# Performance work log

Measured on AMD Instinct MI355X. Metric: run time of the kernel, lower is better.

The kernel has to match this reference:

```python
import jax, jax.numpy as jnp
import numpy as np

N = 80000      # nodes
E = 1280000    # edges
G = 64         # graphs in batch
CIN = 128
D = 64
NUM_LAYERS = 6


def setup_inputs() -> dict:
    key = jax.random.key(0)
    ks = jax.random.split(key, 12)
    s = 0.05
    return {
        "x": jax.random.normal(ks[0], (N, CIN), jnp.float32),
        "edge_index": jax.random.randint(ks[1], (2, E), 0, N, dtype=jnp.int32),
        "batch": jnp.sort(jax.random.randint(ks[2], (N,), 0, G, dtype=jnp.int32)),
        "W_in": jax.random.normal(ks[3], (CIN, D), jnp.float32) * s,
        "b_in": jnp.zeros((D,), jnp.float32),
        "W_hid": jax.random.normal(ks[4], (NUM_LAYERS - 1, D, D), jnp.float32) * s,
        "b_hid": jnp.zeros((NUM_LAYERS - 1, D), jnp.float32),
        "lin1_w": jax.random.normal(ks[5], (2 * D, 64), jnp.float32) * s,
        "lin1_b": jnp.zeros((64,), jnp.float32),
        "lin2_w": jax.random.normal(ks[6], (64, 64), jnp.float32) * s,
        "lin2_b": jnp.zeros((64,), jnp.float32),
        "lin3_w": jax.random.normal(ks[7], (64, 1), jnp.float32) * s,
        "lin3_b": jnp.zeros((1,), jnp.float32),
    }


def _gcn_norm(edge_index, n):
    # PyG gcn_norm: add self-loops, symmetric D^-1/2 (A+I) D^-1/2 normalization
    loops = jnp.arange(n, dtype=edge_index.dtype)
    src = jnp.concatenate([edge_index[0], loops])
    dst = jnp.concatenate([edge_index[1], loops])
    deg = jax.ops.segment_sum(jnp.ones_like(src, jnp.float32), dst, num_segments=n)
    dinv = jnp.where(deg > 0, jax.lax.rsqrt(jnp.maximum(deg, 1.0)), 0.0)
    norm = dinv[src] * dinv[dst]
    return src, dst, norm


def _gcn_conv(x, W, b, src, dst, norm, n):
    h = x @ W                                   # [N, D]
    msg = h[src] * norm[:, None]                # [E+N, D] gather + scale
    out = jax.ops.segment_sum(msg, dst, num_segments=n)
    return out + b


def reference(x, edge_index, batch, W_in, b_in, W_hid, b_hid,
              lin1_w, lin1_b, lin2_w, lin2_b, lin3_w, lin3_b):
    n = x.shape[0]
    src, dst, norm = _gcn_norm(edge_index, n)
    # layer 0: in_channels -> D, then ReLU
    h = jax.nn.relu(_gcn_conv(x, W_in, b_in, src, dst, norm, n))
    # hidden layers: ReLU on all but the last conv
    n_hid = W_hid.shape[0]
    for i in range(n_hid):
        h = _gcn_conv(h, W_hid[i], b_hid[i], src, dst, norm, n)
        if i != n_hid - 1:
            h = jax.nn.relu(h)
    # global add + max pooling per graph
    x1 = jax.ops.segment_sum(h, batch, num_segments=G)   # [G, D]
    x2 = jax.ops.segment_max(h, batch, num_segments=G)   # [G, D]
    g = jnp.concatenate([x1, x2], axis=1)                # [G, 2D]
    g = jax.nn.relu(g @ lin1_w + lin1_b)
    g = jax.nn.relu(g @ lin2_w + lin2_b)
    return g @ lin3_w + lin3_b                           # [G, 1]
```

## Files before the change

kernel.cpp:

```cpp
#include <hip/hip_runtime.h>
#include <hip/hip_bf16.h>
#include <cstdint>
#include <cstddef>


#define FEAT 64

typedef __bf16 bf16_t;
typedef bf16_t bf16x8 __attribute__((ext_vector_type(8)));
typedef float f32x4 __attribute__((ext_vector_type(4)));

static __device__ inline unsigned short f2bf(float f) {
  unsigned u = __float_as_uint(f);
  unsigned r = (u + 0x7FFF + ((u >> 16) & 1)) >> 16;
  return (unsigned short)r;
}
static __device__ inline float bf2f(unsigned short u) {
  return __uint_as_float(((unsigned)u) << 16);
}


__global__ __launch_bounds__(256) void init_kernel(int* deg, int* cursor,
    float* gsum, unsigned int* gmax, int n) {
  int i = blockIdx.x * 256 + threadIdx.x;
  if (i < n) { deg[i] = 0; cursor[i] = 0; }
  if (i < 64 * FEAT) { gsum[i] = 0.f; gmax[i] = 0xFF800000u; }
}

__global__ __launch_bounds__(256) void hist_kernel(const int* __restrict__ dst,
    int* __restrict__ deg, int e, int n) {
  const int slice = blockIdx.x & 7;
  const int lo = slice * (n >> 3);
  const int hi = lo + (n >> 3);
  const int nb = gridDim.x >> 3;
  const int bid = blockIdx.x >> 3;
  for (int i = bid * 256 + threadIdx.x; i < e; i += nb * 256) {
    int d = dst[i];
    if (d >= lo && d < hi) atomicAdd(&deg[d], 1);
  }
}

__global__ __launch_bounds__(256) void dinv_kernel(const int* __restrict__ deg,
    float* __restrict__ dinv, int n) {
  int i = blockIdx.x * 256 + threadIdx.x;
  if (i < n) dinv[i] = rsqrtf((float)(deg[i] + 1));
}

__global__ __launch_bounds__(256) void scan1_kernel(const int* __restrict__ deg,
    int* __restrict__ offs, int* __restrict__ bsums, int n) {
  __shared__ int buf[256];
  int t = threadIdx.x;
  int i = blockIdx.x * 256 + t;
  int v = (i < n) ? deg[i] : 0;
  buf[t] = v;
  __syncthreads();
  for (int off = 1; off < 256; off <<= 1) {
    int add = (t >= off) ? buf[t - off] : 0;
    __syncthreads();
    buf[t] += add;
    __syncthreads();
  }
  if (i < n) offs[i] = buf[t] - v;
  if (t == 255) bsums[blockIdx.x] = buf[255];
}

__global__ __launch_bounds__(512) void scan2_kernel(int* bs, int nb) {
  __shared__ int buf[512];
  int t = threadIdx.x;
  int v = (t < nb) ? bs[t] : 0;
  buf[t] = v;
  __syncthreads();
  for (int off = 1; off < 512; off <<= 1) {
    int add = (t >= off) ? buf[t - off] : 0;
    __syncthreads();
    buf[t] += add;
    __syncthreads();
  }
  if (t < nb) bs[t] = buf[t] - v;
}

__global__ __launch_bounds__(256) void scan3_kernel(int* __restrict__ offs,
    const int* __restrict__ bs, int n) {
  int i = blockIdx.x * 256 + threadIdx.x;
  if (i < n) offs[i] += bs[blockIdx.x];
}

__global__ __launch_bounds__(256) void fill_kernel(const int* __restrict__ src,
    const int* __restrict__ dst, const int* __restrict__ offs,
    int* __restrict__ cursor, int* __restrict__ csr_src, int e, int n) {
  const int slice = blockIdx.x & 7;
  const int lo = slice * (n >> 3);
  const int hi = lo + (n >> 3);
  const int nb = gridDim.x >> 3;
  const int bid = blockIdx.x >> 3;
  for (int i = bid * 256 + threadIdx.x; i < e; i += nb * 256) {
    int d = dst[i];
    if (d >= lo && d < hi) {
      int pos = offs[d] + atomicAdd(&cursor[d], 1);
      csr_src[pos] = src[i];
    }
  }
}

__global__ __launch_bounds__(256) void wprep_kernel(
    const float* __restrict__ W_in, const float* __restrict__ W_hid,
    unsigned short* __restrict__ wf0h, unsigned short* __restrict__ wf0l,
    unsigned short* __restrict__ wfhh, unsigned short* __restrict__ wfhl) {
  int tid = threadIdx.x;
  for (int i = tid; i < 16 * 64 * 8; i += 256) {
    int j = i & 7, l = (i >> 3) & 63, f = i >> 9;
    int q = f & 3, t = f >> 2;
    int k = q * 32 + (l >> 4) * 8 + j, c = t * 16 + (l & 15);
    float w = W_in[k * 64 + c];
    unsigned short hi = f2bf(w);
    wf0h[i] = hi;
    wf0l[i] = f2bf(w - bf2f(hi));
  }
  for (int i = tid; i < 5 * 8 * 64 * 8; i += 256) {
    int j = i & 7, l = (i >> 3) & 63, f = (i >> 9) & 7, m = i >> 12;
    int q = f & 1, t = f >> 1;
    int k = q * 32 + (l >> 4) * 8 + j, c = t * 16 + (l & 15);
    float w = W_hid[(m * 64 + k) * 64 + c];
    unsigned short hi = f2bf(w);
    wfhh[i] = hi;
    wfhl[i] = f2bf(w - bf2f(hi));
  }
}

static __device__ inline void split8(const float4& a, const float4& b,
                                     bf16x8& vh, bf16x8& vl) {
  union { unsigned short us[8]; bf16x8 v; } uh, ul;
  float va[8] = {a.x, a.y, a.z, a.w, b.x, b.y, b.z, b.w};
#pragma unroll
  for (int j = 0; j < 8; ++j) {
    unsigned short hi = f2bf(va[j]);
    uh.us[j] = hi;
    ul.us[j] = f2bf(va[j] - bf2f(hi));
  }
  vh = uh.v; vl = ul.v;
}

__global__ __launch_bounds__(256) void xform0_kernel(
    const float* __restrict__ x, const unsigned short* __restrict__ wf0h,
    const unsigned short* __restrict__ wf0l, const float* __restrict__ dinv,
    unsigned short* __restrict__ tg, int n) {
  const int lane = threadIdx.x & 63;
  const int r = lane & 15, g = lane >> 4;
  const int gw = (blockIdx.x * 256 + threadIdx.x) >> 6;
  const int th = gw & 1;
  const int tile = gw >> 1;
  if (tile >= (n >> 4)) return;

  bf16x8 wh[2][4], wl[2][4];
#pragma unroll
  for (int tt = 0; tt < 2; ++tt)
#pragma unroll
    for (int q = 0; q < 4; ++q) {
      int f = (th * 2 + tt) * 4 + q;
      wh[tt][q] = *reinterpret_cast<const bf16x8*>(&wf0h[(f * 64 + lane) * 8]);
      wl[tt][q] = *reinterpret_cast<const bf16x8*>(&wf0l[(f * 64 + lane) * 8]);
    }

  const int m0 = tile << 4;
  const float* xrow = x + (size_t)(m0 + r) * 128 + g * 8;
  f32x4 acc[2] = {{0.f, 0.f, 0.f, 0.f}, {0.f, 0.f, 0.f, 0.f}};
#pragma unroll
  for (int q = 0; q < 4; ++q) {
    float4 lo4 = *(const float4*)(xrow + q * 32);
    float4 hi4 = *(const float4*)(xrow + q * 32 + 4);
    bf16x8 ah, al;
    split8(lo4, hi4, ah, al);
#pragma unroll
    for (int tt = 0; tt < 2; ++tt) {
      acc[tt] = __builtin_amdgcn_mfma_f32_16x16x32_bf16(ah, wh[tt][q], acc[tt], 0, 0, 0);
      acc[tt] = __builtin_amdgcn_mfma_f32_16x16x32_bf16(al, wh[tt][q], acc[tt], 0, 0, 0);
      acc[tt] = __builtin_amdgcn_mfma_f32_16x16x32_bf16(ah, wl[tt][q], acc[tt], 0, 0, 0);
    }
  }
  float4 dv = *(const float4*)&dinv[m0 + g * 4];
  unsigned short* orow = tg + (size_t)m0 * 64;
#pragma unroll
  for (int tt = 0; tt < 2; ++tt) {
    int c = (th * 2 + tt) * 16 + r;
    orow[(g * 4 + 0) * 64 + c] = f2bf(acc[tt][0] * dv.x);
    orow[(g * 4 + 1) * 64 + c] = f2bf(acc[tt][1] * dv.y);
    orow[(g * 4 + 2) * 64 + c] = f2bf(acc[tt][2] * dv.z);
    orow[(g * 4 + 3) * 64 + c] = f2bf(acc[tt][3] * dv.w);
  }
}

__global__ __launch_bounds__(256) void xform_kernel(
    const float* __restrict__ h, const unsigned short* __restrict__ wflh,
    const unsigned short* __restrict__ wfll, const float* __restrict__ dinv,
    unsigned short* __restrict__ tg, int n) {
  const int lane = threadIdx.x & 63;
  const int r = lane & 15, g = lane >> 4;
  const int tile = (blockIdx.x * 256 + threadIdx.x) >> 6;
  if (tile >= (n >> 4)) return;

  bf16x8 wh[4][2], wl[4][2];
#pragma unroll
  for (int t = 0; t < 4; ++t)
#pragma unroll
    for (int q = 0; q < 2; ++q) {
      int f = t * 2 + q;
      wh[t][q] = *reinterpret_cast<const bf16x8*>(&wflh[(f * 64 + lane) * 8]);
      wl[t][q] = *reinterpret_cast<const bf16x8*>(&wfll[(f * 64 + lane) * 8]);
    }

  const int m0 = tile << 4;
  const float* hrow = h + (size_t)(m0 + r) * 64 + g * 8;
  f32x4 acc[4] = {{0.f, 0.f, 0.f, 0.f}, {0.f, 0.f, 0.f, 0.f},
                  {0.f, 0.f, 0.f, 0.f}, {0.f, 0.f, 0.f, 0.f}};
#pragma unroll
  for (int q = 0; q < 2; ++q) {
    float4 lo4 = *(const float4*)(hrow + q * 32);
    float4 hi4 = *(const float4*)(hrow + q * 32 + 4);
    bf16x8 ah, al;
    split8(lo4, hi4, ah, al);
#pragma unroll
    for (int t = 0; t < 4; ++t) {
      acc[t] = __builtin_amdgcn_mfma_f32_16x16x32_bf16(ah, wh[t][q], acc[t], 0, 0, 0);
      acc[t] = __builtin_amdgcn_mfma_f32_16x16x32_bf16(al, wh[t][q], acc[t], 0, 0, 0);
      acc[t] = __builtin_amdgcn_mfma_f32_16x16x32_bf16(ah, wl[t][q], acc[t], 0, 0, 0);
    }
  }
  float4 dv = *(const float4*)&dinv[m0 + g * 4];
  unsigned short* orow = tg + (size_t)m0 * 64;
#pragma unroll
  for (int t = 0; t < 4; ++t) {
    orow[(g * 4 + 0) * 64 + t * 16 + r] = f2bf(acc[t][0] * dv.x);
    orow[(g * 4 + 1) * 64 + t * 16 + r] = f2bf(acc[t][1] * dv.y);
    orow[(g * 4 + 2) * 64 + t * 16 + r] = f2bf(acc[t][2] * dv.z);
    orow[(g * 4 + 3) * 64 + t * 16 + r] = f2bf(acc[t][3] * dv.w);
  }
}

__global__ __launch_bounds__(256) void agg_mid_kernel(
    const unsigned short* __restrict__ tg_in, const int* __restrict__ csr_src,
    const int* __restrict__ offs, const int* __restrict__ cnt,
    const float* __restrict__ dinv, const float* __restrict__ bias,
    float* __restrict__ h_out, int n) {
  int v = (blockIdx.x * 256 + threadIdx.x) >> 6;
  int lane = threadIdx.x & 63;
  if (v >= n) return;
  float acc = bf2f(tg_in[(size_t)v * 64 + lane]);
  int j = offs[v];
  int end = j + cnt[v];
  for (; j + 7 < end; j += 8) {
    int s0 = csr_src[j + 0], s1 = csr_src[j + 1];
    int s2 = csr_src[j + 2], s3 = csr_src[j + 3];
    int s4 = csr_src[j + 4], s5 = csr_src[j + 5];
    int s6 = csr_src[j + 6], s7 = csr_src[j + 7];
    float t0 = bf2f(tg_in[(size_t)s0 * 64 + lane]);
    float t1 = bf2f(tg_in[(size_t)s1 * 64 + lane]);
    float t2 = bf2f(tg_in[(size_t)s2 * 64 + lane]);
    float t3 = bf2f(tg_in[(size_t)s3 * 64 + lane]);
    float t4 = bf2f(tg_in[(size_t)s4 * 64 + lane]);
    float t5 = bf2f(tg_in[(size_t)s5 * 64 + lane]);
    float t6 = bf2f(tg_in[(size_t)s6 * 64 + lane]);
    float t7 = bf2f(tg_in[(size_t)s7 * 64 + lane]);
    acc += ((t0 + t1) + (t2 + t3)) + ((t4 + t5) + (t6 + t7));
  }
  for (; j < end; ++j)
    acc += bf2f(tg_in[(size_t)csr_src[j] * 64 + lane]);
  h_out[(size_t)v * 64 + lane] = fmaxf(fmaf(dinv[v], acc, bias[lane]), 0.f);
}

__global__ __launch_bounds__(256) void agg_last_kernel(
    const unsigned short* __restrict__ tg_in, const int* __restrict__ csr_src,
    const int* __restrict__ offs, const int* __restrict__ cnt,
    const float* __restrict__ dinv, const float* __restrict__ bias,
    float* __restrict__ h, int n) {
  int v = (blockIdx.x * 256 + threadIdx.x) >> 6;
  int lane = threadIdx.x & 63;
  if (v >= n) return;
  float acc = bf2f(tg_in[(size_t)v * 64 + lane]);
  int j = offs[v];
  int end = j + cnt[v];
  for (; j + 7 < end; j += 8) {
    int s0 = csr_src[j + 0], s1 = csr_src[j + 1];
    int s2 = csr_src[j + 2], s3 = csr_src[j + 3];
    int s4 = csr_src[j + 4], s5 = csr_src[j + 5];
    int s6 = csr_src[j + 6], s7 = csr_src[j + 7];
    float t0 = bf2f(tg_in[(size_t)s0 * 64 + lane]);
    float t1 = bf2f(tg_in[(size_t)s1 * 64 + lane]);
    float t2 = bf2f(tg_in[(size_t)s2 * 64 + lane]);
    float t3 = bf2f(tg_in[(size_t)s3 * 64 + lane]);
    float t4 = bf2f(tg_in[(size_t)s4 * 64 + lane]);
    float t5 = bf2f(tg_in[(size_t)s5 * 64 + lane]);
    float t6 = bf2f(tg_in[(size_t)s6 * 64 + lane]);
    float t7 = bf2f(tg_in[(size_t)s7 * 64 + lane]);
    acc += ((t0 + t1) + (t2 + t3)) + ((t4 + t5) + (t6 + t7));
  }
  for (; j < end; ++j)
    acc += bf2f(tg_in[(size_t)csr_src[j] * 64 + lane]);
  h[(size_t)v * 64 + lane] = fmaf(dinv[v], acc, bias[lane]);
}


__device__ inline void atomic_max_float(float* addr, float val) {
  if (val >= 0.f)
    atomicMax((int*)addr, __float_as_int(val));
  else
    atomicMin((unsigned int*)addr, (unsigned int)__float_as_int(val));
}

#define POOL_CHUNK 128

__global__ __launch_bounds__(256) void pool_kernel(const float* __restrict__ h,
    const int* __restrict__ batch, float* __restrict__ gsum,
    float* __restrict__ gmax, int n) {
  int wave = (blockIdx.x * 256 + threadIdx.x) >> 6;
  int lane = threadIdx.x & 63;
  int start = wave * POOL_CHUNK;
  if (start >= n) return;
  int end = min(start + POOL_CHUNK, n);
  float s = 0.f, m = -INFINITY;
  int cur = batch[start];
  for (int v = start; v < end; ++v) {
    int g = batch[v];
    if (g != cur) {
      atomicAdd(&gsum[cur * 64 + lane], s);
      atomic_max_float(&gmax[cur * 64 + lane], m);
      s = 0.f; m = -INFINITY; cur = g;
    }
    float x = h[(size_t)v * 64 + lane];
    s += x;
    m = fmaxf(m, x);
  }
  atomicAdd(&gsum[cur * 64 + lane], s);
  atomic_max_float(&gmax[cur * 64 + lane], m);
}


__global__ __launch_bounds__(256) void mlp_kernel(const float* __restrict__ gsum,
    const float* __restrict__ gmax, const float* __restrict__ w1,
    const float* __restrict__ b1, const float* __restrict__ w2,
    const float* __restrict__ b2, const float* __restrict__ w3,
    const float* __restrict__ b3, float* __restrict__ out) {
  __shared__ float smem[64 * 128 + 64 * 64];
  float* gg = smem;
  float* z1 = smem + 64 * 128;
  int t = threadIdx.x;
  for (int i = t; i < 64 * 128; i += 256) {
    int g = i >> 7, f = i & 127;
    gg[i] = (f < 64) ? gsum[g * 64 + f] : gmax[g * 64 + (f - 64)];
  }
  __syncthreads();
  for (int i = t; i < 64 * 64; i += 256) {
    int g = i >> 6, j = i & 63;
    float acc = b1[j];
    for (int f = 0; f < 128; ++f) acc = fmaf(gg[(g << 7) + f], w1[f * 64 + j], acc);
    z1[i] = fmaxf(acc, 0.f);
  }
  __syncthreads();
  float* z2 = smem;
  for (int i = t; i < 64 * 64; i += 256) {
    int g = i >> 6, j = i & 63;
    float acc = b2[j];
    for (int f = 0; f < 64; ++f) acc = fmaf(z1[(g << 6) + f], w2[f * 64 + j], acc);
    z2[i] = fmaxf(acc, 0.f);
  }
  __syncthreads();
  if (t < 64) {
    float acc = b3[0];
    for (int j = 0; j < 64; ++j) acc = fmaf(z2[(t << 6) + j], w3[j], acc);
    out[t] = acc;
  }
}


extern "C" void kernel_launch(void* const* d_in, const int* in_sizes, int n_in,
                              void* d_out, int out_size, void* d_ws, size_t ws_size,
                              hipStream_t stream) {
  const float* x      = (const float*)d_in[0];
  const int*   eidx   = (const int*)d_in[1];
  const int*   batch  = (const int*)d_in[2];
  const float* W_in   = (const float*)d_in[3];
  const float* b_in   = (const float*)d_in[4];
  const float* W_hid  = (const float*)d_in[5];
  const float* b_hid  = (const float*)d_in[6];
  const float* lin1_w = (const float*)d_in[7];
  const float* lin1_b = (const float*)d_in[8];
  const float* lin2_w = (const float*)d_in[9];
  const float* lin2_b = (const float*)d_in[10];
  const float* lin3_w = (const float*)d_in[11];
  const float* lin3_b = (const float*)d_in[12];
  float* out = (float*)d_out;

  const int N = in_sizes[2];
  const int E = in_sizes[1] / 2;
  const int CIN = in_sizes[0] / N;
  const int n_hid = in_sizes[5] / (64 * 64);

  const int* src = eidx;
  const int* dst = eidx + E;

  char* ws = (char*)d_ws;
  size_t off = 0;
  auto alloc = [&](size_t bytes) {
    size_t o = off;
    off = (off + bytes + 255) & ~(size_t)255;
    return o;
  };
  int*            deg     = (int*)(ws + alloc((size_t)N * 4));
  int*            cursor  = (int*)(ws + alloc((size_t)N * 4));
  float*          dinv    = (float*)(ws + alloc((size_t)N * 4));
  int*            offs    = (int*)(ws + alloc((size_t)N * 4));
  int*            bsums   = (int*)(ws + alloc(1024 * 4));
  int*            csr_src = (int*)(ws + alloc((size_t)E * 4));
  unsigned short* tg_a    = (unsigned short*)(ws + alloc((size_t)N * 64 * 2));
  unsigned short* tg_b    = (unsigned short*)(ws + alloc((size_t)N * 64 * 2));
  float*          hbuf    = (float*)(ws + alloc((size_t)N * 64 * 4));
  unsigned short* wf0h    = (unsigned short*)(ws + alloc(16 * 64 * 8 * 2));
  unsigned short* wf0l    = (unsigned short*)(ws + alloc(16 * 64 * 8 * 2));
  unsigned short* wfhh    = (unsigned short*)(ws + alloc(5 * 8 * 64 * 8 * 2));
  unsigned short* wfhl    = (unsigned short*)(ws + alloc(5 * 8 * 64 * 8 * 2));
  float*          gsum    = (float*)(ws + alloc(64 * 64 * 4));
  float*          gmax    = (float*)(ws + alloc(64 * 64 * 4));
  (void)ws_size; (void)n_in; (void)out_size; (void)CIN;

  const int nbN = (N + 255) / 256;

  init_kernel<<<nbN, 256, 0, stream>>>(deg, cursor, gsum, (unsigned int*)gmax, N);
  hist_kernel<<<1024, 256, 0, stream>>>(dst, deg, E, N);
  dinv_kernel<<<nbN, 256, 0, stream>>>(deg, dinv, N);
  scan1_kernel<<<nbN, 256, 0, stream>>>(deg, offs, bsums, N);
  scan2_kernel<<<1, 512, 0, stream>>>(bsums, nbN);
  scan3_kernel<<<nbN, 256, 0, stream>>>(offs, bsums, N);
  fill_kernel<<<1024, 256, 0, stream>>>(src, dst, offs, cursor, csr_src, E, N);
  wprep_kernel<<<1, 256, 0, stream>>>(W_in, W_hid, wf0h, wf0l, wfhh, wfhl);

  const int agg_blocks = (N * 64 + 255) / 256;
  const int ntile = N >> 4;
  const int xf0_blocks = (ntile * 2 + 3) / 4;
  const int xf_blocks = (ntile + 3) / 4;

  xform0_kernel<<<xf0_blocks, 256, 0, stream>>>(x, wf0h, wf0l, dinv, tg_a, N);

  unsigned short* cur = tg_a;
  unsigned short* nxt = tg_b;
  for (int k = 0; k < n_hid; ++k) {
    const float* bias_k = (k == 0) ? b_in : (b_hid + (size_t)(k - 1) * 64);
    agg_mid_kernel<<<agg_blocks, 256, 0, stream>>>(
        cur, csr_src, offs, deg, dinv, bias_k, hbuf, N);
    xform_kernel<<<xf_blocks, 256, 0, stream>>>(
        hbuf, wfhh + (size_t)k * 8 * 64 * 8, wfhl + (size_t)k * 8 * 64 * 8,
        dinv, nxt, N);
    unsigned short* t = cur; cur = nxt; nxt = t;
  }
  agg_last_kernel<<<agg_blocks, 256, 0, stream>>>(
      cur, csr_src, offs, deg, dinv, b_hid + (size_t)(n_hid - 1) * 64, hbuf, N);

  const int pool_waves = (N + POOL_CHUNK - 1) / POOL_CHUNK;
  const int pool_blocks = (pool_waves * 64 + 255) / 256;
  pool_kernel<<<pool_blocks, 256, 0, stream>>>(hbuf, batch, gsum, gmax, N);

  mlp_kernel<<<1, 256, 0, stream>>>(gsum, gmax, lin1_w, lin1_b, lin2_w, lin2_b,
                                    lin3_w, lin3_b, out);
}
```

Before: 690.0 us.

## Pad CSR rows to multiples of eight with dummy zero node for vector index loads

Each destination's CSR segment is rounded up to a multiple of eight entries. The padding slots are pre-filled with an index pointing to an extra all-zero feature row appended to each bf16 feature buffer. The aggregation kernels can then load indices as two 16-byte vectors per block of eight and drop the scalar remainder loop. Edge reads in the hist and fill kernels become nontemporal and their grids double in size. In exchange, the CSR array gets larger, a pad kernel has to run, and every padded slot costs a redundant gather of the zero row.

```diff
diff --git a/kernel.cpp b/kernel.cpp
--- a/kernel.cpp
+++ b/kernel.cpp
@@ -9,6 +9,7 @@
 typedef __bf16 bf16_t;
 typedef bf16_t bf16x8 __attribute__((ext_vector_type(8)));
 typedef float f32x4 __attribute__((ext_vector_type(4)));
+typedef int intx4 __attribute__((ext_vector_type(4)));
 
 static __device__ inline unsigned short f2bf(float f) {
   unsigned u = __float_as_uint(f);
@@ -25,6 +26,20 @@
   int i = blockIdx.x * 256 + threadIdx.x;
   if (i < n) { deg[i] = 0; cursor[i] = 0; }
   if (i < 64 * FEAT) { gsum[i] = 0.f; gmax[i] = 0xFF800000u; }
+}
+
+__global__ __launch_bounds__(256) void pad_kernel(int* __restrict__ csr,
+    int e8_4, int nval, unsigned short* __restrict__ tga,
+    unsigned short* __restrict__ tgb, int n) {
+  int i = blockIdx.x * 256 + threadIdx.x;
+  if (i < e8_4) {
+    intx4 v4 = {nval, nval, nval, nval};
+    ((intx4*)csr)[i] = v4;
+  }
+  if (blockIdx.x == 0 && threadIdx.x < 64) {
+    tga[(size_t)n * 64 + threadIdx.x] = 0;
+    tgb[(size_t)n * 64 + threadIdx.x] = 0;
+  }
 }
 
 __global__ __launch_bounds__(256) void hist_kernel(const int* __restrict__ dst,
@@ -35,7 +50,7 @@
   const int nb = gridDim.x >> 3;
   const int bid = blockIdx.x >> 3;
   for (int i = bid * 256 + threadIdx.x; i < e; i += nb * 256) {
-    int d = dst[i];
+    int d = __builtin_nontemporal_load(&dst[i]);
     if (d >= lo && d < hi) atomicAdd(&deg[d], 1);
   }
 }
@@ -51,7 +66,7 @@
   __shared__ int buf[256];
   int t = threadIdx.x;
   int i = blockIdx.x * 256 + t;
-  int v = (i < n) ? deg[i] : 0;
+  int v = (i < n) ? ((deg[i] + 7) & ~7) : 0;
   buf[t] = v;
   __syncthreads();
   for (int off = 1; off < 256; off <<= 1) {
@@ -94,10 +109,11 @@
   const int nb = gridDim.x >> 3;
   const int bid = blockIdx.x >> 3;
   for (int i = bid * 256 + threadIdx.x; i < e; i += nb * 256) {
-    int d = dst[i];
+    int d = __builtin_nontemporal_load(&dst[i]);
     if (d >= lo && d < hi) {
+      int s = __builtin_nontemporal_load(&src[i]);
       int pos = offs[d] + atomicAdd(&cursor[d], 1);
-      csr_src[pos] = src[i];
+      csr_src[pos] = s;
     }
   }
 }
@@ -246,24 +262,20 @@
   if (v >= n) return;
   float acc = bf2f(tg_in[(size_t)v * 64 + lane]);
   int j = offs[v];
-  int end = j + cnt[v];
-  for (; j + 7 < end; j += 8) {
-    int s0 = csr_src[j + 0], s1 = csr_src[j + 1];
-    int s2 = csr_src[j + 2], s3 = csr_src[j + 3];
-    int s4 = csr_src[j + 4], s5 = csr_src[j + 5];
-    int s6 = csr_src[j + 6], s7 = csr_src[j + 7];
-    float t0 = bf2f(tg_in[(size_t)s0 * 64 + lane]);
-    float t1 = bf2f(tg_in[(size_t)s1 * 64 + lane]);
-    float t2 = bf2f(tg_in[(size_t)s2 * 64 + lane]);
-    float t3 = bf2f(tg_in[(size_t)s3 * 64 + lane]);
-    float t4 = bf2f(tg_in[(size_t)s4 * 64 + lane]);
-    float t5 = bf2f(tg_in[(size_t)s5 * 64 + lane]);
-    float t6 = bf2f(tg_in[(size_t)s6 * 64 + lane]);
-    float t7 = bf2f(tg_in[(size_t)s7 * 64 + lane]);
+  int nb = (cnt[v] + 7) >> 3;
+  for (int b = 0; b < nb; ++b, j += 8) {
+    intx4 ia = __builtin_nontemporal_load((const intx4*)(csr_src + j));
+    intx4 ib = __builtin_nontemporal_load((const intx4*)(csr_src + j + 4));
+    float t0 = bf2f(tg_in[(size_t)ia.x * 64 + lane]);
+    float t1 = bf2f(tg_in[(size_t)ia.y * 64 + lane]);
+    float t2 = bf2f(tg_in[(size_t)ia.z * 64 + lane]);
+    float t3 = bf2f(tg_in[(size_t)ia.w * 64 + lane]);
+    float t4 = bf2f(tg_in[(size_t)ib.x * 64 + lane]);
+    float t5 = bf2f(tg_in[(size_t)ib.y * 64 + lane]);
+    float t6 = bf2f(tg_in[(size_t)ib.z * 64 + lane]);
+    float t7 = bf2f(tg_in[(size_t)ib.w * 64 + lane]);
     acc += ((t0 + t1) + (t2 + t3)) + ((t4 + t5) + (t6 + t7));
   }
-  for (; j < end; ++j)
-    acc += bf2f(tg_in[(size_t)csr_src[j] * 64 + lane]);
   h_out[(size_t)v * 64 + lane] = fmaxf(fmaf(dinv[v], acc, bias[lane]), 0.f);
 }
 
@@ -277,24 +289,20 @@
   if (v >= n) return;
   float acc = bf2f(tg_in[(size_t)v * 64 + lane]);
   int j = offs[v];
-  int end = j + cnt[v];
-  for (; j + 7 < end; j += 8) {
-    int s0 = csr_src[j + 0], s1 = csr_src[j + 1];
-    int s2 = csr_src[j + 2], s3 = csr_src[j + 3];
-    int s4 = csr_src[j + 4], s5 = csr_src[j + 5];
-    int s6 = csr_src[j + 6], s7 = csr_src[j + 7];
-    float t0 = bf2f(tg_in[(size_t)s0 * 64 + lane]);
-    float t1 = bf2f(tg_in[(size_t)s1 * 64 + lane]);
-    float t2 = bf2f(tg_in[(size_t)s2 * 64 + lane]);
-    float t3 = bf2f(tg_in[(size_t)s3 * 64 + lane]);
-    float t4 = bf2f(tg_in[(size_t)s4 * 64 + lane]);
-    float t5 = bf2f(tg_in[(size_t)s5 * 64 + lane]);
-    float t6 = bf2f(tg_in[(size_t)s6 * 64 + lane]);
-    float t7 = bf2f(tg_in[(size_t)s7 * 64 + lane]);
+  int nb = (cnt[v] + 7) >> 3;
+  for (int b = 0; b < nb; ++b, j += 8) {
+    intx4 ia = __builtin_nontemporal_load((const intx4*)(csr_src + j));
+    intx4 ib = __builtin_nontemporal_load((const intx4*)(csr_src + j + 4));
+    float t0 = bf2f(tg_in[(size_t)ia.x * 64 + lane]);
+    float t1 = bf2f(tg_in[(size_t)ia.y * 64 + lane]);
+    float t2 = bf2f(tg_in[(size_t)ia.z * 64 + lane]);
+    float t3 = bf2f(tg_in[(size_t)ia.w * 64 + lane]);
+    float t4 = bf2f(tg_in[(size_t)ib.x * 64 + lane]);
+    float t5 = bf2f(tg_in[(size_t)ib.y * 64 + lane]);
+    float t6 = bf2f(tg_in[(size_t)ib.z * 64 + lane]);
+    float t7 = bf2f(tg_in[(size_t)ib.w * 64 + lane]);
     acc += ((t0 + t1) + (t2 + t3)) + ((t4 + t5) + (t6 + t7));
   }
-  for (; j < end; ++j)
-    acc += bf2f(tg_in[(size_t)csr_src[j] * 64 + lane]);
   h[(size_t)v * 64 + lane] = fmaf(dinv[v], acc, bias[lane]);
 }
 
@@ -397,6 +405,8 @@
   const int* src = eidx;
   const int* dst = eidx + E;
 
+  const int E8 = E + 8 * N;
+
   char* ws = (char*)d_ws;
   size_t off = 0;
   auto alloc = [&](size_t bytes) {
@@ -409,9 +419,9 @@
   float*          dinv    = (float*)(ws + alloc((size_t)N * 4));
   int*            offs    = (int*)(ws + alloc((size_t)N * 4));
   int*            bsums   = (int*)(ws + alloc(1024 * 4));
-  int*            csr_src = (int*)(ws + alloc((size_t)E * 4));
-  unsigned short* tg_a    = (unsigned short*)(ws + alloc((size_t)N * 64 * 2));
-  unsigned short* tg_b    = (unsigned short*)(ws + alloc((size_t)N * 64 * 2));
+  int*            csr_src = (int*)(ws + alloc((size_t)E8 * 4));
+  unsigned short* tg_a    = (unsigned short*)(ws + alloc((size_t)(N + 1) * 64 * 2));
+  unsigned short* tg_b    = (unsigned short*)(ws + alloc((size_t)(N + 1) * 64 * 2));
   float*          hbuf    = (float*)(ws + alloc((size_t)N * 64 * 4));
   unsigned short* wf0h    = (unsigned short*)(ws + alloc(16 * 64 * 8 * 2));
   unsigned short* wf0l    = (unsigned short*)(ws + alloc(16 * 64 * 8 * 2));
@@ -422,14 +432,16 @@
   (void)ws_size; (void)n_in; (void)out_size; (void)CIN;
 
   const int nbN = (N + 255) / 256;
+  const int e8_4 = E8 / 4;
 
   init_kernel<<<nbN, 256, 0, stream>>>(deg, cursor, gsum, (unsigned int*)gmax, N);
-  hist_kernel<<<1024, 256, 0, stream>>>(dst, deg, E, N);
+  pad_kernel<<<(e8_4 + 255) / 256, 256, 0, stream>>>(csr_src, e8_4, N, tg_a, tg_b, N);
+  hist_kernel<<<2048, 256, 0, stream>>>(dst, deg, E, N);
   dinv_kernel<<<nbN, 256, 0, stream>>>(deg, dinv, N);
   scan1_kernel<<<nbN, 256, 0, stream>>>(deg, offs, bsums, N);
   scan2_kernel<<<1, 512, 0, stream>>>(bsums, nbN);
   scan3_kernel<<<nbN, 256, 0, stream>>>(offs, bsums, N);
-  fill_kernel<<<1024, 256, 0, stream>>>(src, dst, offs, cursor, csr_src, E, N);
+  fill_kernel<<<2048, 256, 0, stream>>>(src, dst, offs, cursor, csr_src, E, N);
   wprep_kernel<<<1, 256, 0, stream>>>(W_in, W_hid, wf0h, wf0l, wfhh, wfhl);
 
   const int agg_blocks = (N * 64 + 255) / 256;
```

Measured after the change: 665.7 us. 1.04x faster.
